# Optimization experiments

Hardware: AMD Instinct MI355X
Metric: run time of the kernel (lower is better)

Reference implementation:

```python
import jax, jax.numpy as jnp
import numpy as np

EMBEDS = 195  # C, also used in the (unusual) 1/sqrt(C) scale


def setup_inputs() -> dict:
    key = jax.random.key(0)
    k1, k2, k3, k4 = jax.random.split(key, 4)
    B, T, C, H = 1024, 256, EMBEDS, 8
    x = jax.random.normal(k1, (B, T, C), dtype=jnp.float32)
    Wq = jax.random.normal(k2, (C, H), dtype=jnp.float32) * 0.05
    Wk = jax.random.normal(k3, (C, H), dtype=jnp.float32) * 0.05
    Wv = jax.random.normal(k4, (C, H), dtype=jnp.float32) * 0.05
    return {"x": x, "Wq": Wq, "Wk": Wk, "Wv": Wv}


def reference(x, Wq, Wk, Wv):
    B, T, C = x.shape
    q = jnp.einsum('btc,ch->bth', x, Wq)  # [B,T,H]
    k = jnp.einsum('btc,ch->bth', x, Wk)
    v = jnp.einsum('btc,ch->bth', x, Wv)
    # scores scaled by 1/sqrt(C) (embedding dim), faithful to source
    scores = jnp.einsum('bqh,bkh->bqk', q, k) * (1.0 / jnp.sqrt(jnp.float32(C)))
    causal = jnp.tril(jnp.ones((T, T), dtype=bool))  # [T,T]
    scores = jnp.where(causal, scores, -jnp.inf)
    attn = jax.nn.softmax(scores, axis=-1)
    # dropout treated as identity (eval mode) for deterministic reference
    out = jnp.einsum('bqk,bkh->bqh', attn, v)
    return out
```

## Files before the change

kernel.cpp:

```cpp
#include <hip/hip_runtime.h>
#include <hip/hip_bf16.h>
#include <stdint.h>

#define TT   256
#define CC   195
#define HH   8
#define NKT  7
#define VSTR 260
#define PSTR 40

typedef __attribute__((ext_vector_type(8))) short short8;
typedef __attribute__((ext_vector_type(4))) float f32x4;

static __device__ __forceinline__ short f2bf(float v) {
    union { __hip_bfloat16 h; short s; } cv;
    cv.h = __float2bfloat16(v);
    return cv.s;
}

__global__ __launch_bounds__(256, 4)
void fused_head(const float* __restrict__ x,
                const float* __restrict__ Wq,
                const float* __restrict__ Wk,
                const float* __restrict__ Wv,
                float* __restrict__ out)
{
    __shared__ short Ql[TT * 8];
    __shared__ short Kl[TT * 8];
    __shared__ short Vt[16 * VSTR];
    __shared__ short Pch[4 * 16 * PSTR];

    const int tid  = threadIdx.x;
    const int lane = tid & 63;
    const int wv   = __builtin_amdgcn_readfirstlane(tid >> 6);
    const int b    = blockIdx.x;
    const int nn   = lane & 15;
    const int quad = lane >> 4;

    {
        uint32_t* vtw = (uint32_t*)Vt;
        const int base = (8 * VSTR) / 2;
        for (int i = tid; i < (8 * VSTR) / 2; i += 256)
            vtw[base + i] = (i < VSTR / 2) ? 0x3F803F80u : 0u;
    }

    const float* __restrict__ xb = x + (size_t)b * (TT * CC);

    const float* Wsel0 = (nn < 8) ? (Wq + nn) : (Wk + nn - 8);
    const float* Wsel1 = (nn < 8) ? (Wv + nn) : nullptr;
    short8 Bf[NKT][2];
#pragma unroll
    for (int kt = 0; kt < NKT; ++kt) {
#pragma unroll
        for (int j = 0; j < 8; ++j) {
            const int k = kt * 32 + quad * 8 + j;
            float v0 = (k < CC) ? Wsel0[(size_t)k * HH] : 0.f;
            float v1 = (k < CC && Wsel1) ? Wsel1[(size_t)k * HH] : 0.f;
            Bf[kt][0][j] = f2bf(v0);
            Bf[kt][1][j] = f2bf(v1);
        }
    }

    for (int ch = 0; ch < 4; ++ch) {
        const int rbase = ch * 64 + wv * 16;
        const float* __restrict__ xrow = xb + (size_t)(rbase + nn) * CC;

        f32x4 acc0 = {0.f, 0.f, 0.f, 0.f};
        f32x4 acc1 = {0.f, 0.f, 0.f, 0.f};
#pragma unroll
        for (int kt = 0; kt < NKT; ++kt) {
            float f[8];
#pragma unroll
            for (int j = 0; j < 8; ++j) {
                const int k = kt * 32 + quad * 8 + j;
                f[j] = (k < CC) ? xrow[k] : 0.f;
            }
            short8 a;
#pragma unroll
            for (int j = 0; j < 8; ++j) a[j] = f2bf(f[j]);
            acc0 = __builtin_amdgcn_mfma_f32_16x16x32_bf16(a, Bf[kt][0], acc0, 0, 0, 0);
            acc1 = __builtin_amdgcn_mfma_f32_16x16x32_bf16(a, Bf[kt][1], acc1, 0, 0, 0);
        }
#pragma unroll
        for (int r = 0; r < 4; ++r) {
            const int trow = rbase + quad * 4 + r;
            const short qs = f2bf(acc0[r]);
            if (nn < 8) {
                Ql[trow * 8 + nn] = qs;
                Vt[nn * VSTR + trow] = f2bf(acc1[r]);
            } else {
                Kl[trow * 8 + (nn - 8)] = qs;
            }
        }
    }
    __syncthreads();

    const float SC2 = 0.07161149f * 1.44269504f;
    const int qt4[4] = { wv, 7 - wv, 8 + wv, 15 - wv };
    short* Pw = Pch + wv * (16 * PSTR);

    for (int qi = 0; qi < 4; ++qi) {
        const int qt = qt4[qi];
        const int qb = qt * 16;

        short8 aQ = (short8){0, 0, 0, 0, 0, 0, 0, 0};
        if (quad == 0)
            aQ = *reinterpret_cast<const short8*>(Ql + (qb + nn) * 8);

        f32x4 accO = {0.f, 0.f, 0.f, 0.f};
        const int nch = (qt >> 1) + 1;
        for (int c = 0; c < nch; ++c) {
            const int kb = c * 32;
            asm volatile("" ::: "memory");
#pragma unroll
            for (int half = 0; half < 2; ++half) {
                const int kb16 = kb + half * 16;
                short8 bK = (short8){0, 0, 0, 0, 0, 0, 0, 0};
                if (quad == 0)
                    bK = *reinterpret_cast<const short8*>(Kl + (kb16 + nn) * 8);
                f32x4 s = __builtin_amdgcn_mfma_f32_16x16x32_bf16(
                              aQ, bK, (f32x4){0.f, 0.f, 0.f, 0.f}, 0, 0, 0);
                const int key = kb16 + nn;
#pragma unroll
                for (int r = 0; r < 4; ++r) {
                    const int qrow = qb + quad * 4 + r;
                    const float e = (key <= qrow) ? exp2f(s[r] * SC2) : 0.f;
                    Pw[(quad * 4 + r) * PSTR + half * 16 + nn] = f2bf(e);
                }
            }
            asm volatile("s_waitcnt lgkmcnt(0)" ::: "memory");
            const short8 aP = *reinterpret_cast<const short8*>(Pw + nn * PSTR + quad * 8);
            const short8 bV = *reinterpret_cast<const short8*>(Vt + nn * VSTR + kb + quad * 8);
            accO = __builtin_amdgcn_mfma_f32_16x16x32_bf16(aP, bV, accO, 0, 0, 0);
        }
#pragma unroll
        for (int r = 0; r < 4; ++r) {
            const float dn = __shfl(accO[r], (lane & 48) | 8);
            if (nn < 8) {
                const int qrow = qb + quad * 4 + r;
                out[((size_t)b * TT + qrow) * HH + nn] = accO[r] / dn;
            }
        }
    }
}

extern "C" void kernel_launch(void* const* d_in, const int* in_sizes, int n_in,
                              void* d_out, int out_size, void* d_ws, size_t ws_size,
                              hipStream_t stream)
{
    const float* x  = (const float*)d_in[0];
    const float* Wq = (const float*)d_in[1];
    const float* Wk = (const float*)d_in[2];
    const float* Wv = (const float*)d_in[3];
    float* out      = (float*)d_out;
    const int B = in_sizes[0] / (TT * CC);
    fused_head<<<dim3(B), dim3(256), 0, stream>>>(x, Wq, Wk, Wv, out);
}
```

Measured before the change: 306.5 us.

## Compute transposed scores to keep P in registers, skip masked half-tiles

Swaps the operand order of the QK^T MFMA so each lane's score output already matches the A-operand layout of the PV MFMA. The probability tile can then be packed in registers instead of going through a per-wave LDS staging buffer with a waitcnt. V is gathered as two 4-element pieces to match the permuted key ordering. The second 16-key half is skipped on the diagonal chunk when it is fully masked. This removes LDS round trips and a sync point per chunk, at the cost of more scattered V loads and some extra branching.

```diff
diff --git a/kernel.cpp b/kernel.cpp
--- a/kernel.cpp
+++ b/kernel.cpp
@@ -7,9 +7,9 @@
 #define HH   8
 #define NKT  7
 #define VSTR 260
-#define PSTR 40
 
 typedef __attribute__((ext_vector_type(8))) short short8;
+typedef __attribute__((ext_vector_type(4))) short short4v;
 typedef __attribute__((ext_vector_type(4))) float f32x4;
 
 static __device__ __forceinline__ short f2bf(float v) {
@@ -28,7 +28,6 @@
     __shared__ short Ql[TT * 8];
     __shared__ short Kl[TT * 8];
     __shared__ short Vt[16 * VSTR];
-    __shared__ short Pch[4 * 16 * PSTR];
 
     const int tid  = threadIdx.x;
     const int lane = tid & 63;
@@ -97,48 +96,61 @@
 
     const float SC2 = 0.07161149f * 1.44269504f;
     const int qt4[4] = { wv, 7 - wv, 8 + wv, 15 - wv };
-    short* Pw = Pch + wv * (16 * PSTR);
 
     for (int qi = 0; qi < 4; ++qi) {
         const int qt = qt4[qi];
         const int qb = qt * 16;
+        const int qcol = qb + nn;
 
-        short8 aQ = (short8){0, 0, 0, 0, 0, 0, 0, 0};
+        short8 bQ = (short8){0, 0, 0, 0, 0, 0, 0, 0};
         if (quad == 0)
-            aQ = *reinterpret_cast<const short8*>(Ql + (qb + nn) * 8);
+            bQ = *reinterpret_cast<const short8*>(Ql + (qb + nn) * 8);
 
         f32x4 accO = {0.f, 0.f, 0.f, 0.f};
         const int nch = (qt >> 1) + 1;
         for (int c = 0; c < nch; ++c) {
             const int kb = c * 32;
-            asm volatile("" ::: "memory");
+            const bool doH1 = (c < nch - 1) || (qt & 1);
+
+            short8 aK0 = (short8){0, 0, 0, 0, 0, 0, 0, 0};
+            short8 aK1 = (short8){0, 0, 0, 0, 0, 0, 0, 0};
+            if (quad == 0) {
+                aK0 = *reinterpret_cast<const short8*>(Kl + (kb + nn) * 8);
+                if (doH1)
+                    aK1 = *reinterpret_cast<const short8*>(Kl + (kb + 16 + nn) * 8);
+            }
+            f32x4 s0 = __builtin_amdgcn_mfma_f32_16x16x32_bf16(
+                           aK0, bQ, (f32x4){0.f, 0.f, 0.f, 0.f}, 0, 0, 0);
+            f32x4 s1 = {0.f, 0.f, 0.f, 0.f};
+            if (doH1)
+                s1 = __builtin_amdgcn_mfma_f32_16x16x32_bf16(
+                         aK1, bQ, (f32x4){0.f, 0.f, 0.f, 0.f}, 0, 0, 0);
+
+            const short* vrow = Vt + nn * VSTR + kb + quad * 4;
+            const short4v v0 = *reinterpret_cast<const short4v*>(vrow);
+            const short4v v1 = *reinterpret_cast<const short4v*>(vrow + 16);
+
+            const int keyb = kb + quad * 4;
+            short8 aP, bV;
 #pragma unroll
-            for (int half = 0; half < 2; ++half) {
-                const int kb16 = kb + half * 16;
-                short8 bK = (short8){0, 0, 0, 0, 0, 0, 0, 0};
-                if (quad == 0)
-                    bK = *reinterpret_cast<const short8*>(Kl + (kb16 + nn) * 8);
-                f32x4 s = __builtin_amdgcn_mfma_f32_16x16x32_bf16(
-                              aQ, bK, (f32x4){0.f, 0.f, 0.f, 0.f}, 0, 0, 0);
-                const int key = kb16 + nn;
-#pragma unroll
-                for (int r = 0; r < 4; ++r) {
-                    const int qrow = qb + quad * 4 + r;
-                    const float e = (key <= qrow) ? exp2f(s[r] * SC2) : 0.f;
-                    Pw[(quad * 4 + r) * PSTR + half * 16 + nn] = f2bf(e);
-                }
+            for (int r = 0; r < 4; ++r) {
+                const float e0 = (keyb + r <= qcol) ? exp2f(s0[r] * SC2) : 0.f;
+                const float e1 = (doH1 && (keyb + 16 + r <= qcol))
+                                     ? exp2f(s1[r] * SC2) : 0.f;
+                aP[r]     = f2bf(e0);
+                aP[4 + r] = f2bf(e1);
+                bV[r]     = v0[r];
+                bV[4 + r] = v1[r];
             }
-            asm volatile("s_waitcnt lgkmcnt(0)" ::: "memory");
-            const short8 aP = *reinterpret_cast<const short8*>(Pw + nn * PSTR + quad * 8);
-            const short8 bV = *reinterpret_cast<const short8*>(Vt + nn * VSTR + kb + quad * 8);
             accO = __builtin_amdgcn_mfma_f32_16x16x32_bf16(aP, bV, accO, 0, 0, 0);
         }
+
 #pragma unroll
         for (int r = 0; r < 4; ++r) {
             const float dn = __shfl(accO[r], (lane & 48) | 8);
             if (nn < 8) {
-                const int qrow = qb + quad * 4 + r;
-                out[((size_t)b * TT + qrow) * HH + nn] = accO[r] / dn;
+                const int q = qb + quad * 4 + r;
+                out[((size_t)b * TT + q) * HH + nn] = accO[r] / dn;
             }
         }
     }
```

After: 306.2 us. About the same (-0.1%).
